# Kernel optimization log

Measured on AMD Instinct MI355X. Metric: run time of the kernel, lower is better.

The kernel has to match this reference:

```python
import jax, jax.numpy as jnp
import numpy as np

B, S, D, H = 2, 2048, 1024, 16
DK = D // H


def setup_inputs() -> dict:
    key = jax.random.key(0)
    ks = jax.random.split(key, 6)
    scale = D ** -0.5
    return {
        "x": jax.random.normal(ks[0], (B, S, D), dtype=jnp.float32),
        "Wq": jax.random.normal(ks[1], (D, D), dtype=jnp.float32) * scale,
        "Wk": jax.random.normal(ks[2], (D, D), dtype=jnp.float32) * scale,
        "Wv": jax.random.normal(ks[3], (D, D), dtype=jnp.float32) * scale,
        "Wp": jax.random.normal(ks[4], (D, D), dtype=jnp.float32) * scale,
        "bp": jax.random.normal(ks[5], (D,), dtype=jnp.float32) * 0.01,
    }


def reference(x, Wq, Wk, Wv, Wp, bp):
    b, s, d = x.shape
    # projections (torch Linear: x @ W.T)
    q = (x @ Wq.T).reshape(b, s, H, DK).transpose(0, 2, 1, 3)  # [b,h,s,dk]
    k = (x @ Wk.T).reshape(b, s, H, DK).transpose(0, 2, 1, 3)
    v = (x @ Wv.T).reshape(b, s, H, DK).transpose(0, 2, 1, 3)
    wei = jnp.einsum('bhqd,bhkd->bhqk', q, k) * (DK ** -0.5)  # [b,h,s,s]
    causal = jnp.tril(jnp.ones((s, s), dtype=bool))
    wei = jnp.where(causal, wei, -jnp.inf)
    wei = jax.nn.softmax(wei, axis=-1)
    out = jnp.einsum('bhqk,bhkd->bhqd', wei, v)
    out = out.transpose(0, 2, 1, 3).reshape(b, s, H * DK)
    return out @ Wp.T + bp
```

## Files before the change

kernel.cpp:

```cpp
#include <hip/hip_runtime.h>

typedef short short8 __attribute__((ext_vector_type(8)));
typedef float floatx4 __attribute__((ext_vector_type(4)));
typedef float floatx16 __attribute__((ext_vector_type(16)));

#define DEV static __device__ __forceinline__

DEV unsigned short f2bf(float x) {
    union { float f; unsigned u; } v; v.f = x;
    unsigned r = v.u + 0x7FFFu + ((v.u >> 16) & 1u);
    return (unsigned short)(r >> 16);
}

DEV unsigned pk2(float lo, float hi) {
    return (unsigned)f2bf(lo) | ((unsigned)f2bf(hi) << 16);
}

DEV __attribute__((address_space(3))) unsigned int* lds_as3(void* p) {
    return (__attribute__((address_space(3))) unsigned int*)(unsigned int)(unsigned long long)p;
}
DEV const __attribute__((address_space(1))) unsigned int* gbl_as1(const void* p) {
    return (const __attribute__((address_space(1))) unsigned int*)(unsigned long long)p;
}

__global__ __launch_bounds__(256) void cvt_all(
    const float* __restrict__ x,  const float* __restrict__ wq,
    const float* __restrict__ wk, const float* __restrict__ wv,
    const float* __restrict__ wp,
    unsigned short* __restrict__ xb, unsigned short* __restrict__ wqkv,
    unsigned short* __restrict__ wpb)
{
    long c = (long)blockIdx.x * 256 + threadIdx.x;
    const float* src; unsigned short* dst; long off;
    if      (c <  524288) { src = x;  dst = xb;             off = c;          }
    else if (c <  655360) { src = wq; dst = wqkv;           off = c - 524288; }
    else if (c <  786432) { src = wk; dst = wqkv + 1048576; off = c - 655360; }
    else if (c <  917504) { src = wv; dst = wqkv + 2097152; off = c - 786432; }
    else                  { src = wp; dst = wpb;            off = c - 917504; }
    float4 a = ((const float4*)src)[off * 2];
    float4 b = ((const float4*)src)[off * 2 + 1];
    ushort4 r0, r1;
    r0.x = f2bf(a.x); r0.y = f2bf(a.y); r0.z = f2bf(a.z); r0.w = f2bf(a.w);
    r1.x = f2bf(b.x); r1.y = f2bf(b.y); r1.z = f2bf(b.z); r1.w = f2bf(b.w);
    ((ushort4*)dst)[off * 2]     = r0;
    ((ushort4*)dst)[off * 2 + 1] = r1;
}

template <int EPI>
__global__ __launch_bounds__(256) void gemm_bt(
    const unsigned short* __restrict__ A, const unsigned short* __restrict__ Bw,
    int M, int N, int K,
    unsigned short* __restrict__ Qd, unsigned short* __restrict__ Kd,
    unsigned short* __restrict__ Vtd,
    float* __restrict__ Cout, const float* __restrict__ bias)
{
    __shared__ unsigned short As[128 * 32];
    __shared__ unsigned short Bs[128 * 32];
    const int t    = threadIdx.x;
    const int lane = t & 63;
    const int wv   = t >> 6;
    const int wr   = (wv >> 1) * 64, wc = (wv & 1) * 64;
    const int lr   = lane & 15,      lg = lane >> 4;
    const int m0   = blockIdx.y * 128, n0 = blockIdx.x * 128;
    const int trow = t >> 2;
    const int tk   = (t & 3) * 8;

    floatx4 acc[4][4];
#pragma unroll
    for (int i = 0; i < 4; ++i)
#pragma unroll
        for (int j = 0; j < 4; ++j)
#pragma unroll
            for (int r = 0; r < 4; ++r) acc[i][j][r] = 0.f;

    for (int k0 = 0; k0 < K; k0 += 32) {
        __syncthreads();
#pragma unroll
        for (int r = 0; r < 2; ++r) {
            const unsigned short* ga = A  + (size_t)(m0 + r * 64 + trow) * K + k0 + tk;
            const unsigned short* gb = Bw + (size_t)(n0 + r * 64 + trow) * K + k0 + tk;
            __builtin_amdgcn_global_load_lds(gbl_as1(ga), lds_as3(&As[(r * 256 + t) * 8]), 16, 0, 0);
            __builtin_amdgcn_global_load_lds(gbl_as1(gb), lds_as3(&Bs[(r * 256 + t) * 8]), 16, 0, 0);
        }
        __syncthreads();
        short8 af[4], bf[4];
#pragma unroll
        for (int i = 0; i < 4; ++i) {
            af[i] = *(const short8*)&As[(wr + i * 16 + lr) * 32 + lg * 8];
            bf[i] = *(const short8*)&Bs[(wc + i * 16 + lr) * 32 + lg * 8];
        }
#pragma unroll
        for (int i = 0; i < 4; ++i)
#pragma unroll
            for (int j = 0; j < 4; ++j)
                acc[i][j] = __builtin_amdgcn_mfma_f32_16x16x32_bf16(af[i], bf[j], acc[i][j], 0, 0, 0);
    }

    if (EPI == 1) {
#pragma unroll
        for (int j = 0; j < 4; ++j) {
            int n = n0 + wc + j * 16 + lr;
            float bv = bias[n];
#pragma unroll
            for (int i = 0; i < 4; ++i) {
                int mb = m0 + wr + i * 16 + lg * 4;
#pragma unroll
                for (int r = 0; r < 4; ++r)
                    Cout[(size_t)(mb + r) * N + n] = acc[i][j][r] + bv;
            }
        }
    } else {
        const int which = n0 >> 10;
#pragma unroll
        for (int j = 0; j < 4; ++j) {
            int n = n0 + wc + j * 16 + lr;
            int h = (n & 1023) >> 6, d = n & 63;
#pragma unroll
            for (int i = 0; i < 4; ++i) {
                int mb = m0 + wr + i * 16 + lg * 4;
                int b = mb >> 11, s0 = mb & 2047;
                size_t bh = (size_t)(b * 16 + h);
                if (which == 2) {
                    ushort4 pv;
                    pv.x = f2bf(acc[i][j][0]); pv.y = f2bf(acc[i][j][1]);
                    pv.z = f2bf(acc[i][j][2]); pv.w = f2bf(acc[i][j][3]);
                    *(ushort4*)&Vtd[(bh * 64 + d) * 2048 + s0] = pv;
                } else {
                    unsigned short* dst = (which ? Kd : Qd) + (bh * 2048 + s0) * 64 + d;
#pragma unroll
                    for (int r = 0; r < 4; ++r) dst[r * 64] = f2bf(acc[i][j][r]);
                }
            }
        }
    }
}

__global__ __launch_bounds__(256) void attn_fwd(
    const unsigned short* __restrict__ Q, const unsigned short* __restrict__ Kg,
    const unsigned short* __restrict__ Vt, unsigned short* __restrict__ O)
{
    __shared__ unsigned short ot[4][32][80];
    const int bh = blockIdx.x;
    const int qt = blockIdx.y;
    const int t  = threadIdx.x, w = t >> 6, l = t & 63;
    const int lq = l & 31, hh = l >> 5;
    const int qw = qt * 128 + w * 32;
    const unsigned short* Qp = Q  + (size_t)bh * 2048 * 64;
    const unsigned short* Kp = Kg + (size_t)bh * 2048 * 64;
    const unsigned short* Vp = Vt + (size_t)bh * 64 * 2048;

    short8 qf[4];
#pragma unroll
    for (int kk = 0; kk < 4; ++kk)
        qf[kk] = *(const short8*)&Qp[(qw + lq) * 64 + kk * 16 + hh * 8];

    floatx16 o0, o1;
#pragma unroll
    for (int r = 0; r < 16; ++r) { o0[r] = 0.f; o1[r] = 0.f; }
    float mrun = -1e30f, lrun = 0.f;

    for (int kv0 = 0; kv0 <= qw; kv0 += 32) {
        floatx16 sa;
#pragma unroll
        for (int r = 0; r < 16; ++r) sa[r] = 0.f;
#pragma unroll
        for (int kk = 0; kk < 4; ++kk) {
            short8 kf = *(const short8*)&Kp[(kv0 + lq) * 64 + kk * 16 + hh * 8];
            sa = __builtin_amdgcn_mfma_f32_32x32x16_bf16(kf, qf[kk], sa, 0, 0, 0);
        }
        float sv[16];
        float tm = -1e30f;
#pragma unroll
        for (int r = 0; r < 16; ++r) {
            int crow = (r & 3) + 8 * (r >> 2) + 4 * hh;
            float xx = sa[r] * 0.125f;
            if (kv0 + crow > qw + lq) xx = -1e30f;
            sv[r] = xx;
            tm = fmaxf(tm, xx);
        }
        tm = fmaxf(tm, __shfl_xor(tm, 32));
        float mn = fmaxf(mrun, tm);
        float f  = __expf(mrun - mn);
        float ps = 0.f;
#pragma unroll
        for (int r = 0; r < 16; ++r) { sv[r] = __expf(sv[r] - mn); ps += sv[r]; }
        ps += __shfl_xor(ps, 32);
        lrun = lrun * f + ps;
        mrun = mn;
#pragma unroll
        for (int r = 0; r < 16; ++r) { o0[r] *= f; o1[r] *= f; }

#pragma unroll
        for (int c = 0; c < 2; ++c) {
            unsigned a0 = pk2(sv[c*8+0], sv[c*8+1]);
            unsigned a1 = pk2(sv[c*8+2], sv[c*8+3]);
            unsigned b0 = pk2(sv[c*8+4], sv[c*8+5]);
            unsigned b1 = pk2(sv[c*8+6], sv[c*8+7]);
            unsigned sa0 = __shfl_xor(a0, 32), sa1 = __shfl_xor(a1, 32);
            unsigned sb0 = __shfl_xor(b0, 32), sb1 = __shfl_xor(b1, 32);
            union { unsigned u[4]; short8 v; } pf;
            pf.u[0] = hh ? sb0 : a0;
            pf.u[1] = hh ? sb1 : a1;
            pf.u[2] = hh ? b0  : sa0;
            pf.u[3] = hh ? b1  : sa1;
            short8 vf0 = *(const short8*)&Vp[(size_t)(lq)      * 2048 + kv0 + c * 16 + hh * 8];
            short8 vf1 = *(const short8*)&Vp[(size_t)(32 + lq) * 2048 + kv0 + c * 16 + hh * 8];
            o0 = __builtin_amdgcn_mfma_f32_32x32x16_bf16(vf0, pf.v, o0, 0, 0, 0);
            o1 = __builtin_amdgcn_mfma_f32_32x32x16_bf16(vf1, pf.v, o1, 0, 0, 0);
        }
    }

    float inv = 1.f / lrun;
#pragma unroll
    for (int r = 0; r < 16; ++r) {
        int crow = (r & 3) + 8 * (r >> 2) + 4 * hh;
        ot[w][lq][crow]      = f2bf(o0[r] * inv);
        ot[w][lq][32 + crow] = f2bf(o1[r] * inv);
    }
    asm volatile("s_waitcnt lgkmcnt(0)" ::: "memory");
    const int b = bh >> 4, h = bh & 15;
    const int row = l >> 1, part = l & 1;
    size_t obase = (size_t)(b * 2048 + qt * 128 + w * 32 + row) * 1024 + h * 64 + part * 32;
#pragma unroll
    for (int jj = 0; jj < 4; ++jj) {
        uint4 v = *(const uint4*)&ot[w][row][part * 32 + jj * 8];
        *(uint4*)&O[obase + jj * 8] = v;
    }
}

extern "C" void kernel_launch(void* const* d_in, const int* in_sizes, int n_in,
                              void* d_out, int out_size, void* d_ws, size_t ws_size,
                              hipStream_t stream)
{
    const float* x  = (const float*)d_in[0];
    const float* Wq = (const float*)d_in[1];
    const float* Wk = (const float*)d_in[2];
    const float* Wv = (const float*)d_in[3];
    const float* Wp = (const float*)d_in[4];
    const float* bp = (const float*)d_in[5];
    float* out = (float*)d_out;

    char* ws = (char*)d_ws;
    unsigned short* xb   = (unsigned short*)(ws);
    unsigned short* wqkv = (unsigned short*)(ws + 8388608);
    unsigned short* wpb  = (unsigned short*)(ws + 14680064);
    unsigned short* Qw   = (unsigned short*)(ws + 16777216);
    unsigned short* Kw   = (unsigned short*)(ws + 25165824);
    unsigned short* Vtw  = (unsigned short*)(ws + 33554432);
    unsigned short* Ow   = (unsigned short*)(ws + 41943040);

    cvt_all<<<4096, 256, 0, stream>>>(x, Wq, Wk, Wv, Wp, xb, wqkv, wpb);
    gemm_bt<0><<<dim3(24, 32), 256, 0, stream>>>(xb, wqkv, 4096, 3072, 1024,
                                                 Qw, Kw, Vtw, nullptr, nullptr);
    attn_fwd<<<dim3(32, 16), 256, 0, stream>>>(Qw, Kw, Vtw, Ow);
    gemm_bt<1><<<dim3(8, 32), 256, 0, stream>>>(Ow, wpb, 4096, 1024, 1024,
                                                nullptr, nullptr, nullptr, out, bp);
}
```

Before: 235.2 us.

## Streamline attention softmax with exp2, lazy rescaling, diagonal-only masking and reversed tiles

Folds log2(e) into the score scale so exponentials use the hardware exp2 directly. The causal mask is applied only on the diagonal tile. Rescaling of the running output is skipped unless the row max grows by more than a threshold (FA4-style lazy rescale). The bf16 packing uses the HIP intrinsic, and query tiles are launched in reverse order so the longest causal blocks start first. Together these cut VALU work in the softmax inner loop and improve load balance, at the cost of slightly larger unnormalized intermediate values.

```diff
diff --git a/kernel.cpp b/kernel.cpp
--- a/kernel.cpp
+++ b/kernel.cpp
@@ -1,4 +1,5 @@
 #include <hip/hip_runtime.h>
+#include <hip/hip_bf16.h>
 
 typedef short short8 __attribute__((ext_vector_type(8)));
 typedef float floatx4 __attribute__((ext_vector_type(4)));
@@ -13,7 +14,17 @@
 }
 
 DEV unsigned pk2(float lo, float hi) {
-    return (unsigned)f2bf(lo) | ((unsigned)f2bf(hi) << 16);
+    union { __hip_bfloat162 h; unsigned u; } v;
+    v.h = __float22bfloat162_rn(make_float2(lo, hi));
+    return v.u;
+}
+
+DEV float fexp2(float x) {
+#if __has_builtin(__builtin_amdgcn_exp2f)
+    return __builtin_amdgcn_exp2f(x);
+#else
+    return exp2f(x);
+#endif
 }
 
 DEV __attribute__((address_space(3))) unsigned int* lds_as3(void* p) {
@@ -141,7 +152,7 @@
 {
     __shared__ unsigned short ot[4][32][80];
     const int bh = blockIdx.x;
-    const int qt = blockIdx.y;
+    const int qt = 15 - blockIdx.y;
     const int t  = threadIdx.x, w = t >> 6, l = t & 63;
     const int lq = l & 31, hh = l >> 5;
     const int qw = qt * 128 + w * 32;
@@ -149,6 +160,8 @@
     const unsigned short* Kp = Kg + (size_t)bh * 2048 * 64;
     const unsigned short* Vp = Vt + (size_t)bh * 64 * 2048;
 
+    const float SCALE2 = 0.18033688011112042f;
+
     short8 qf[4];
 #pragma unroll
     for (int kk = 0; kk < 4; ++kk)
@@ -170,25 +183,37 @@
         }
         float sv[16];
         float tm = -1e30f;
-#pragma unroll
-        for (int r = 0; r < 16; ++r) {
-            int crow = (r & 3) + 8 * (r >> 2) + 4 * hh;
-            float xx = sa[r] * 0.125f;
-            if (kv0 + crow > qw + lq) xx = -1e30f;
-            sv[r] = xx;
-            tm = fmaxf(tm, xx);
+        if (kv0 == qw) {
+#pragma unroll
+            for (int r = 0; r < 16; ++r) {
+                int crow = (r & 3) + 8 * (r >> 2) + 4 * hh;
+                float xx = sa[r] * SCALE2;
+                if (crow > lq) xx = -1e30f;
+                sv[r] = xx;
+                tm = fmaxf(tm, xx);
+            }
+        } else {
+#pragma unroll
+            for (int r = 0; r < 16; ++r) {
+                float xx = sa[r] * SCALE2;
+                sv[r] = xx;
+                tm = fmaxf(tm, xx);
+            }
         }
         tm = fmaxf(tm, __shfl_xor(tm, 32));
-        float mn = fmaxf(mrun, tm);
-        float f  = __expf(mrun - mn);
+        if (!__all(tm - mrun <= 8.f)) {
+            float mn = fmaxf(mrun, tm);
+            float f  = fexp2(mrun - mn);
+            lrun *= f;
+#pragma unroll
+            for (int r = 0; r < 16; ++r) { o0[r] *= f; o1[r] *= f; }
+            mrun = mn;
+        }
         float ps = 0.f;
 #pragma unroll
-        for (int r = 0; r < 16; ++r) { sv[r] = __expf(sv[r] - mn); ps += sv[r]; }
+        for (int r = 0; r < 16; ++r) { sv[r] = fexp2(sv[r] - mrun); ps += sv[r]; }
         ps += __shfl_xor(ps, 32);
-        lrun = lrun * f + ps;
-        mrun = mn;
-#pragma unroll
-        for (int r = 0; r < 16; ++r) { o0[r] *= f; o1[r] *= f; }
+        lrun += ps;
 
 #pragma unroll
         for (int c = 0; c < 2; ++c) {
```

New measurement: 234.9 us. About the same (-0.1%).
